# Performance work log

Measured on AMD Instinct MI355X. Metric: run time of the kernel, lower is better.

The kernel has to match this reference:

```python
import jax, jax.numpy as jnp
import numpy as np

B, S, D = 2, 2048, 1024
E, K, DFF = 8, 2, 4 * 1024
EPS_GATE = 1e-8
EPS_LN = 1e-5


def setup_inputs() -> dict:
    key = jax.random.key(0)
    ks = jax.random.split(key, 4)
    scaled = lambda k, shape, fan: (jax.random.normal(k, shape, jnp.float32) / np.sqrt(fan).astype(np.float32))
    return {
        "x": jax.random.normal(ks[0], (B, S, D), jnp.float32),
        "Wg": scaled(ks[1], (D, E), D),
        "bg": jnp.zeros((E,), jnp.float32),
        "W1": scaled(ks[2], (E, D, DFF), D),
        "b1": jnp.zeros((E, DFF), jnp.float32),
        "W2": scaled(ks[3], (E, DFF, D), DFF),
        "b2": jnp.zeros((E, D), jnp.float32),
        "gamma": jnp.ones((D,), jnp.float32),
        "beta": jnp.zeros((D,), jnp.float32),
    }


def reference(x, Wg, bg, W1, b1, W2, b2, gamma, beta):
    b, s, d = x.shape
    xf = x.reshape(-1, d)                       # [T, D]
    T = xf.shape[0]
    num_experts = Wg.shape[1]

    # Gating: softmax over experts, top-k, renormalize selected weights.
    logits = xf @ Wg + bg                       # [T, E]
    w = jax.nn.softmax(logits, axis=-1)
    top_w, top_idx = jax.lax.top_k(w, K)        # [T, K]
    top_w = top_w / (top_w.sum(axis=-1, keepdims=True) + EPS_GATE)

    # Dense combine weights: cw[t, e] = renormalized weight if e selected else 0.
    cw = jnp.zeros((T, num_experts), xf.dtype).at[
        jnp.arange(T)[:, None], top_idx].add(top_w)

    # Expert FFNs (loop over small fixed expert count), weighted combine.
    out = jnp.zeros_like(xf)
    for e in range(num_experts):
        h = jax.nn.gelu(xf @ W1[e] + b1[e], approximate=False)  # [T, DFF]
        y = h @ W2[e] + b2[e]                                    # [T, D]
        out = out + cw[:, e:e + 1] * y

    # LayerNorm over the whole combined output (as in the torch module).
    mu = out.mean(axis=-1, keepdims=True)
    var = out.var(axis=-1, keepdims=True)
    out = (out - mu) / jnp.sqrt(var + EPS_LN) * gamma + beta
    return out.reshape(b, s, d)
```

## Files before the change

### kernel.cpp

```cpp
#include <hip/hip_runtime.h>
#include <hip/hip_bf16.h>

#define TOK  4096
#define DIMD 1024
#define NEXP 8
#define DFFN 4096
#define NSLOT   (TOK*2 + NEXP*128)
#define NRB128  ((TOK*2)/128 + NEXP)

typedef __attribute__((ext_vector_type(8))) short bf16x8;
typedef __attribute__((ext_vector_type(4))) float f32x4;

__device__ __forceinline__ unsigned short f2bf(float f){
  unsigned int u = __float_as_uint(f);
  unsigned int r = u + 0x7FFFu + ((u >> 16) & 1u);
  return (unsigned short)(r >> 16);
}

__device__ __forceinline__ float bf2f(unsigned short h){
  unsigned int u = ((unsigned int)h) << 16;
  return __uint_as_float(u);
}

__device__ __forceinline__ void gload_lds16(const void* g, void* l){
  __builtin_amdgcn_global_load_lds(
      (const __attribute__((address_space(1))) unsigned int*)g,
      (__attribute__((address_space(3))) unsigned int*)l, 16, 0, 0);
}

__global__ __launch_bounds__(256) void k_gate_tr(
    const float* __restrict__ x, const float* __restrict__ Wg,
    const float* __restrict__ bg, int* __restrict__ topidx,
    float* __restrict__ topw, int* __restrict__ pos, int* __restrict__ count,
    unsigned short* __restrict__ xb,
    const float* __restrict__ W1, unsigned short* __restrict__ w1t,
    const float* __restrict__ W2, unsigned short* __restrict__ w2t)
{
  if (blockIdx.x < 4096){
    int bid = blockIdx.x;
    const float* I; unsigned short* O; int R, C, r0, c0;
    if (bid < 2048){
      const int e = bid >> 8, rem = bid & 255;
      R = DIMD; C = DFFN;
      I = W1 + (size_t)e * R * C; O = w1t + (size_t)e * R * C;
      r0 = (rem >> 5) * 128; c0 = (rem & 31) * 128;
    } else {
      bid -= 2048;
      const int e = bid >> 8, rem = bid & 255;
      R = DFFN; C = DIMD;
      I = W2 + (size_t)e * R * C; O = w2t + (size_t)e * R * C;
      r0 = (rem >> 3) * 128; c0 = (rem & 7) * 128;
    }
    __shared__ alignas(16) unsigned short tile[128*128];
    const int tid = threadIdx.x;
    const int qw = tid & 31;
    const int rw = tid >> 5;
    #pragma unroll
    for (int it = 0; it < 16; ++it){
      const int r = it * 8 + rw;
      const float4 v = *(const float4*)(I + (size_t)(r0 + r) * C + c0 + qw * 4);
      ushort4 o;
      o.x = f2bf(v.x); o.y = f2bf(v.y); o.z = f2bf(v.z); o.w = f2bf(v.w);
      const int slot = qw ^ ((r >> 2) & 31);
      *(ushort4*)&tile[r * 128 + slot * 4] = o;
    }
    __syncthreads();
    const int p  = tid & 31;
    const int cb = tid >> 5;
    #pragma unroll
    for (int it = 0; it < 4; ++it){
      const int cg = cb * 4 + it;
      const int sl = (cg ^ p) * 4;
      const ushort4 a0 = *(const ushort4*)&tile[(4*p + 0) * 128 + sl];
      const ushort4 a1 = *(const ushort4*)&tile[(4*p + 1) * 128 + sl];
      const ushort4 a2 = *(const ushort4*)&tile[(4*p + 2) * 128 + sl];
      const ushort4 a3 = *(const ushort4*)&tile[(4*p + 3) * 128 + sl];
      ushort4 o;
      o.x = a0.x; o.y = a1.x; o.z = a2.x; o.w = a3.x;
      *(ushort4*)(O + (size_t)(c0 + 4*cg + 0) * R + r0 + 4*p) = o;
      o.x = a0.y; o.y = a1.y; o.z = a2.y; o.w = a3.y;
      *(ushort4*)(O + (size_t)(c0 + 4*cg + 1) * R + r0 + 4*p) = o;
      o.x = a0.z; o.y = a1.z; o.z = a2.z; o.w = a3.z;
      *(ushort4*)(O + (size_t)(c0 + 4*cg + 2) * R + r0 + 4*p) = o;
      o.x = a0.w; o.y = a1.w; o.z = a2.w; o.w = a3.w;
      *(ushort4*)(O + (size_t)(c0 + 4*cg + 3) * R + r0 + 4*p) = o;
    }
    return;
  }
  const int gb = blockIdx.x - 4096;
  const int wid = threadIdx.x >> 6, lane = threadIdx.x & 63;
  const int t = gb * 4 + wid;
  const float* xr = x + (size_t)t * DIMD;
  unsigned short* xbr = xb + (size_t)t * DIMD;
  float acc[NEXP] = {0.f,0.f,0.f,0.f,0.f,0.f,0.f,0.f};
  #pragma unroll
  for (int j = 0; j < DIMD/64; ++j){
    const int d = j*64 + lane;
    const float xv = xr[d];
    xbr[d] = f2bf(xv);
    const float4 wa = *(const float4*)(Wg + (size_t)d*NEXP);
    const float4 wb = *(const float4*)(Wg + (size_t)d*NEXP + 4);
    acc[0] += xv*wa.x; acc[1] += xv*wa.y; acc[2] += xv*wa.z; acc[3] += xv*wa.w;
    acc[4] += xv*wb.x; acc[5] += xv*wb.y; acc[6] += xv*wb.z; acc[7] += xv*wb.w;
  }
  #pragma unroll
  for (int e = 0; e < NEXP; ++e){
    float v = acc[e];
    #pragma unroll
    for (int o = 32; o > 0; o >>= 1) v += __shfl_xor(v, o);
    acc[e] = v;
  }
  if (lane == 0){
    float lg[NEXP], m = -1e30f;
    #pragma unroll
    for (int e = 0; e < NEXP; ++e){ lg[e] = acc[e] + bg[e]; m = fmaxf(m, lg[e]); }
    float p[NEXP], S = 0.f;
    #pragma unroll
    for (int e = 0; e < NEXP; ++e){ p[e] = expf(lg[e] - m); S += p[e]; }
    int e0 = 0;
    #pragma unroll
    for (int e = 1; e < NEXP; ++e) if (p[e] > p[e0]) e0 = e;
    int e1 = (e0 == 0) ? 1 : 0;
    #pragma unroll
    for (int e = 0; e < NEXP; ++e){
      if (e == e0 || e == e1) continue;
      if (p[e] > p[e1]) e1 = e;
    }
    const float denom = p[e0] + p[e1] + 1e-8f * S;
    const float w0 = p[e0] / denom, w1 = p[e1] / denom;
    const int p0 = atomicAdd(&count[e0], 1);
    const int p1 = atomicAdd(&count[e1], 1);
    topidx[t*2] = e0; topidx[t*2+1] = e1;
    topw[t*2] = w0;   topw[t*2+1] = w1;
    pos[t*2] = p0;    pos[t*2+1] = p1;
  }
}

__global__ __launch_bounds__(256) void k_scatter(
    const int* __restrict__ topidx, const int* __restrict__ pos,
    const int* __restrict__ count, int* __restrict__ slot_of, int* __restrict__ tok_of)
{
  int basee[NEXP]; int bacc = 0;
  #pragma unroll
  for (int q = 0; q < NEXP; ++q){
    basee[q] = bacc << 7;
    bacc += (count[q] + 127) >> 7;
  }
  const int t = blockIdx.x * 256 + threadIdx.x;
  #pragma unroll
  for (int k = 0; k < 2; ++k){
    const int e = topidx[t*2+k];
    const int g = basee[e] + pos[t*2+k];
    slot_of[t*2+k] = g;
    tok_of[g] = t;
  }
}

template<int KD, int KSLICES, int NT, int MODE, int WAVES, int BM, int BN, int MINW>
__global__ __launch_bounds__(WAVES*64, MINW) void k_gemm(
    const unsigned short* __restrict__ A, const unsigned short* __restrict__ Bt,
    const float* __restrict__ bias, const int* __restrict__ tok_of,
    const int* __restrict__ count,
    unsigned short* __restrict__ outH, unsigned short* __restrict__ outY,
    unsigned short* __restrict__ outY1)
{
  const int by = blockIdx.y;
  int e = -1, b0 = 0;
  #pragma unroll
  for (int q = 0; q < NEXP; ++q){
    const int nb = (count[q] + 127) >> 7;
    if (e < 0){ if (by < b0 + nb) e = q; else b0 += nb; }
  }
  if (e < 0) return;
  const int ct = blockIdx.x;
  const int ks = (KSLICES == 1) ? 0 : blockIdx.z;
  constexpr int KSL = KD / KSLICES;
  const int kbase = ks * KSL;
  const int row0 = by * 128;
  constexpr int T   = WAVES * 64;
  constexpr int RA  = BM*8 / T;
  constexpr int RB  = BN*8 / T;
  constexpr int WN  = BN / 64;
  constexpr int WM  = WAVES / WN;
  constexpr int MR  = BM / WM / 16;
  __shared__ alignas(16) unsigned short sA[BM*64];
  __shared__ alignas(16) unsigned short sB[BN*64];
  const int tid = threadIdx.x, wid = tid >> 6, lane = tid & 63;

  const unsigned short* aptr[RA];
  #pragma unroll
  for (int i = 0; i < RA; ++i){
    const int s = i*T + tid;
    const int row = s >> 3;
    const int c = (s & 7) ^ (row & 7);
    size_t arow;
    if (MODE == 1) arow = (size_t)tok_of[row0 + row] * KD;
    else           arow = (size_t)(row0 + row) * KD;
    aptr[i] = A + arow + kbase + c*8;
  }
  const unsigned short* bptr[RB];
  #pragma unroll
  for (int i = 0; i < RB; ++i){
    const int s = i*T + tid;
    const int row = s >> 3;
    const int c = (s & 7) ^ (row & 7);
    bptr[i] = Bt + ((size_t)e*NT + ct*BN + row) * KD + kbase + c*8;
  }

  f32x4 acc[MR][4] = {};
  const int wr = wid / WN, wc = wid % WN;

  int aoff[MR][2], boff[4][2];
  #pragma unroll
  for (int m = 0; m < MR; ++m){
    #pragma unroll
    for (int s = 0; s < 2; ++s){
      const int rowA = wr*(MR*16) + m*16 + (lane & 15);
      aoff[m][s] = rowA*64 + (((s*4) + (lane >> 4)) ^ (rowA & 7))*8;
    }
  }
  #pragma unroll
  for (int n = 0; n < 4; ++n){
    #pragma unroll
    for (int s = 0; s < 2; ++s){
      const int rowB = wc*64 + n*16 + (lane & 15);
      boff[n][s] = rowB*64 + (((s*4) + (lane >> 4)) ^ (rowB & 7))*8;
    }
  }

  for (int k0 = 0; k0 < KSL; k0 += 64){
    #pragma unroll
    for (int i = 0; i < RA; ++i)
      gload_lds16(aptr[i] + k0, &sA[(i*T + tid - lane)*8]);
    #pragma unroll
    for (int i = 0; i < RB; ++i)
      gload_lds16(bptr[i] + k0, &sB[(i*T + tid - lane)*8]);
    __syncthreads();
    #pragma unroll
    for (int s = 0; s < 2; ++s){
      bf16x8 af[MR], bfr[4];
      #pragma unroll
      for (int m = 0; m < MR; ++m) af[m] = *(const bf16x8*)&sA[aoff[m][s]];
      #pragma unroll
      for (int n = 0; n < 4; ++n) bfr[n] = *(const bf16x8*)&sB[boff[n][s]];
      #pragma unroll
      for (int m = 0; m < MR; ++m)
        #pragma unroll
        for (int n = 0; n < 4; ++n)
          acc[m][n] = __builtin_amdgcn_mfma_f32_16x16x32_bf16(af[m], bfr[n], acc[m][n], 0, 0, 0);
    }
    __syncthreads();
  }

  const float* be = bias + (size_t)e * NT;
  unsigned short* outYs = (ks == 0) ? outY : outY1;
  #pragma unroll
  for (int m = 0; m < MR; ++m){
    #pragma unroll
    for (int n = 0; n < 4; ++n){
      #pragma unroll
      for (int j = 0; j < 4; ++j){
        const int rl = wr*(MR*16) + m*16 + ((lane >> 4) << 2) + j;
        const int ng = ct*BN + wc*64 + n*16 + (lane & 15);
        const size_t orow = (size_t)(row0 + rl) * NT + ng;
        if (MODE == 1){
          const float u = acc[m][n][j] + be[ng];
          float y = 0.7978845608028654f * (u + 0.044715f * u * u * u);
          y = fminf(fmaxf(y, -15.f), 15.f);
          const float ex = __expf(2.f * y);
          const float th = (ex - 1.f) / (ex + 1.f);
          outH[orow] = f2bf(0.5f * u * (1.f + th));
        } else {
          outYs[orow] = f2bf(acc[m][n][j] + ((ks == 0) ? be[ng] : 0.f));
        }
      }
    }
  }
}

__global__ __launch_bounds__(256) void k_combine_ln(
    const unsigned short* __restrict__ Ys0, const unsigned short* __restrict__ Ys1,
    const int* __restrict__ slot_of,
    const float* __restrict__ topw, const float* __restrict__ gamma,
    const float* __restrict__ beta, float* __restrict__ out)
{
  const int t = blockIdx.x;
  const int g0 = slot_of[t*2], g1 = slot_of[t*2+1];
  const float w0 = topw[t*2], w1 = topw[t*2+1];
  const int c = threadIdx.x;
  const ushort4 a0 = *(const ushort4*)(Ys0 + (size_t)g0*DIMD + c*4);
  const ushort4 a1 = *(const ushort4*)(Ys1 + (size_t)g0*DIMD + c*4);
  const ushort4 b0 = *(const ushort4*)(Ys0 + (size_t)g1*DIMD + c*4);
  const ushort4 b1 = *(const ushort4*)(Ys1 + (size_t)g1*DIMD + c*4);
  float4 v;
  v.x = w0*(bf2f(a0.x)+bf2f(a1.x)) + w1*(bf2f(b0.x)+bf2f(b1.x));
  v.y = w0*(bf2f(a0.y)+bf2f(a1.y)) + w1*(bf2f(b0.y)+bf2f(b1.y));
  v.z = w0*(bf2f(a0.z)+bf2f(a1.z)) + w1*(bf2f(b0.z)+bf2f(b1.z));
  v.w = w0*(bf2f(a0.w)+bf2f(a1.w)) + w1*(bf2f(b0.w)+bf2f(b1.w));
  float s  = v.x + v.y + v.z + v.w;
  float ss = v.x*v.x + v.y*v.y + v.z*v.z + v.w*v.w;
  #pragma unroll
  for (int o = 32; o > 0; o >>= 1){ s += __shfl_xor(s, o); ss += __shfl_xor(ss, o); }
  __shared__ float red[8];
  const int wid = threadIdx.x >> 6, lane = threadIdx.x & 63;
  if (lane == 0){ red[wid] = s; red[4 + wid] = ss; }
  __syncthreads();
  const float S  = red[0] + red[1] + red[2] + red[3];
  const float SS = red[4] + red[5] + red[6] + red[7];
  const float mu  = S * (1.f/DIMD);
  const float var = SS * (1.f/DIMD) - mu*mu;
  const float inv = rsqrtf(var + 1e-5f);
  const float4 gm = *(const float4*)(gamma + c*4);
  const float4 bt = *(const float4*)(beta + c*4);
  float4 o;
  o.x = (v.x - mu)*inv*gm.x + bt.x;
  o.y = (v.y - mu)*inv*gm.y + bt.y;
  o.z = (v.z - mu)*inv*gm.z + bt.z;
  o.w = (v.w - mu)*inv*gm.w + bt.w;
  *(float4*)(out + (size_t)t*DIMD + c*4) = o;
}

extern "C" void kernel_launch(void* const* d_in, const int* in_sizes, int n_in,
                              void* d_out, int out_size, void* d_ws, size_t ws_size,
                              hipStream_t stream)
{
  const float* x     = (const float*)d_in[0];
  const float* Wg    = (const float*)d_in[1];
  const float* bg    = (const float*)d_in[2];
  const float* W1    = (const float*)d_in[3];
  const float* b1    = (const float*)d_in[4];
  const float* W2    = (const float*)d_in[5];
  const float* b2    = (const float*)d_in[6];
  const float* gamma = (const float*)d_in[7];
  const float* beta  = (const float*)d_in[8];
  float* out = (float*)d_out;

  char* ws = (char*)d_ws;
  size_t off = 0;
  auto alloc = [&](size_t b){ char* p = ws + off; off += (b + 255) & ~(size_t)255; return p; };
  unsigned short* xb  = (unsigned short*)alloc((size_t)TOK*DIMD*2);
  unsigned short* w1t = (unsigned short*)alloc((size_t)NEXP*DFFN*DIMD*2);
  unsigned short* w2t = (unsigned short*)alloc((size_t)NEXP*DIMD*DFFN*2);
  unsigned short* Hs  = (unsigned short*)alloc((size_t)NSLOT*DFFN*2);
  int*   topidx  = (int*)alloc(TOK*2*4);
  float* topw    = (float*)alloc(TOK*2*4);
  int*   pos     = (int*)alloc(TOK*2*4);
  int*   slot_of = (int*)alloc(TOK*2*4);
  int*   tok_of  = (int*)alloc(NSLOT*4);
  int*   count   = (int*)alloc(256);
  unsigned short* Ys0b = (unsigned short*)w1t;
  unsigned short* Ys1b = Ys0b + (size_t)NSLOT*DIMD;

  (void)hipMemsetAsync(count, 0, NEXP*sizeof(int), stream);
  (void)hipMemsetAsync(tok_of, 0, NSLOT*sizeof(int), stream);
  k_gate_tr<<<5120, 256, 0, stream>>>(x, Wg, bg, topidx, topw, pos, count, xb,
                                      W1, w1t, W2, w2t);
  k_scatter<<<TOK/256, 256, 0, stream>>>(topidx, pos, count, slot_of, tok_of);
  k_gemm<DIMD, 1, DFFN, 1, 8, 128, 256, 4><<<dim3(DFFN/256, NRB128), 512, 0, stream>>>(
      xb, w1t, b1, tok_of, count, Hs, nullptr, nullptr);
  k_gemm<DFFN, 2, DIMD, 2, 8, 128, 256, 4><<<dim3(DIMD/256, NRB128, 2), 512, 0, stream>>>(
      Hs, w2t, b2, tok_of, count, nullptr, Ys0b, Ys1b);
  k_combine_ln<<<TOK, 256, 0, stream>>>(Ys0b, Ys1b, slot_of, topw, gamma, beta, out);
}
```

Before: 409.6 us.

## Move W2 transpose-convert into first expert GEMM launch as extra blocks

```diff
diff --git a/kernel.cpp b/kernel.cpp
--- a/kernel.cpp
+++ b/kernel.cpp
@@ -28,29 +28,20 @@
       (__attribute__((address_space(3))) unsigned int*)l, 16, 0, 0);
 }
 
-__global__ __launch_bounds__(256) void k_gate_tr(
+__global__ __launch_bounds__(256) void k_gate_trw1(
     const float* __restrict__ x, const float* __restrict__ Wg,
     const float* __restrict__ bg, int* __restrict__ topidx,
     float* __restrict__ topw, int* __restrict__ pos, int* __restrict__ count,
     unsigned short* __restrict__ xb,
-    const float* __restrict__ W1, unsigned short* __restrict__ w1t,
-    const float* __restrict__ W2, unsigned short* __restrict__ w2t)
-{
-  if (blockIdx.x < 4096){
-    int bid = blockIdx.x;
-    const float* I; unsigned short* O; int R, C, r0, c0;
-    if (bid < 2048){
-      const int e = bid >> 8, rem = bid & 255;
-      R = DIMD; C = DFFN;
-      I = W1 + (size_t)e * R * C; O = w1t + (size_t)e * R * C;
-      r0 = (rem >> 5) * 128; c0 = (rem & 31) * 128;
-    } else {
-      bid -= 2048;
-      const int e = bid >> 8, rem = bid & 255;
-      R = DFFN; C = DIMD;
-      I = W2 + (size_t)e * R * C; O = w2t + (size_t)e * R * C;
-      r0 = (rem >> 3) * 128; c0 = (rem & 7) * 128;
-    }
+    const float* __restrict__ W1, unsigned short* __restrict__ w1t)
+{
+  if (blockIdx.x < 2048){
+    const int bid = blockIdx.x;
+    const int e = bid >> 8, rem = bid & 255;
+    const int R = DIMD, C = DFFN;
+    const float* I = W1 + (size_t)e * R * C;
+    unsigned short* O = w1t + (size_t)e * R * C;
+    const int r0 = (rem >> 5) * 128, c0 = (rem & 31) * 128;
     __shared__ alignas(16) unsigned short tile[128*128];
     const int tid = threadIdx.x;
     const int qw = tid & 31;
@@ -87,7 +78,7 @@
     }
     return;
   }
-  const int gb = blockIdx.x - 4096;
+  const int gb = blockIdx.x - 2048;
   const int wid = threadIdx.x >> 6, lane = threadIdx.x & 63;
   const int t = gb * 4 + wid;
   const float* xr = x + (size_t)t * DIMD;
@@ -156,15 +147,60 @@
   }
 }
 
-template<int KD, int KSLICES, int NT, int MODE, int WAVES, int BM, int BN, int MINW>
+template<int KD, int KSLICES, int NT, int MODE, int WAVES, int BM, int BN, int MINW, int TRW2>
 __global__ __launch_bounds__(WAVES*64, MINW) void k_gemm(
     const unsigned short* __restrict__ A, const unsigned short* __restrict__ Bt,
     const float* __restrict__ bias, const int* __restrict__ tok_of,
     const int* __restrict__ count,
     unsigned short* __restrict__ outH, unsigned short* __restrict__ outY,
-    unsigned short* __restrict__ outY1)
-{
+    unsigned short* __restrict__ outY1,
+    const float* __restrict__ W2src, unsigned short* __restrict__ w2tdst)
+{
+  __shared__ alignas(16) unsigned short smem[BM*64 + BN*64];
   const int by = blockIdx.y;
+
+  if (TRW2 && by >= NRB128){
+    const int bid = (by - NRB128) * gridDim.x + blockIdx.x;
+    const int eT = bid >> 8, rem = bid & 255;
+    const int R = DFFN, C = DIMD;
+    const float* I = W2src + (size_t)eT * R * C;
+    unsigned short* O = w2tdst + (size_t)eT * R * C;
+    const int r0 = (rem >> 3) * 128, c0 = (rem & 7) * 128;
+    unsigned short* tile = smem;
+    const int tid = threadIdx.x;
+    const int qw = tid & 31, rw = tid >> 5;
+    #pragma unroll
+    for (int it = 0; it < 8; ++it){
+      const int r = it * 16 + rw;
+      const float4 v = *(const float4*)(I + (size_t)(r0 + r) * C + c0 + qw * 4);
+      ushort4 o;
+      o.x = f2bf(v.x); o.y = f2bf(v.y); o.z = f2bf(v.z); o.w = f2bf(v.w);
+      const int slot = qw ^ ((r >> 2) & 31);
+      *(ushort4*)&tile[r * 128 + slot * 4] = o;
+    }
+    __syncthreads();
+    const int p = tid & 31, cb = tid >> 5;
+    #pragma unroll
+    for (int it = 0; it < 2; ++it){
+      const int cg = cb * 2 + it;
+      const int sl = (cg ^ p) * 4;
+      const ushort4 a0 = *(const ushort4*)&tile[(4*p + 0) * 128 + sl];
+      const ushort4 a1 = *(const ushort4*)&tile[(4*p + 1) * 128 + sl];
+      const ushort4 a2 = *(const ushort4*)&tile[(4*p + 2) * 128 + sl];
+      const ushort4 a3 = *(const ushort4*)&tile[(4*p + 3) * 128 + sl];
+      ushort4 o;
+      o.x = a0.x; o.y = a1.x; o.z = a2.x; o.w = a3.x;
+      *(ushort4*)(O + (size_t)(c0 + 4*cg + 0) * R + r0 + 4*p) = o;
+      o.x = a0.y; o.y = a1.y; o.z = a2.y; o.w = a3.y;
+      *(ushort4*)(O + (size_t)(c0 + 4*cg + 1) * R + r0 + 4*p) = o;
+      o.x = a0.z; o.y = a1.z; o.z = a2.z; o.w = a3.z;
+      *(ushort4*)(O + (size_t)(c0 + 4*cg + 2) * R + r0 + 4*p) = o;
+      o.x = a0.w; o.y = a1.w; o.z = a2.w; o.w = a3.w;
+      *(ushort4*)(O + (size_t)(c0 + 4*cg + 3) * R + r0 + 4*p) = o;
+    }
+    return;
+  }
+
   int e = -1, b0 = 0;
   #pragma unroll
   for (int q = 0; q < NEXP; ++q){
@@ -183,8 +219,8 @@
   constexpr int WN  = BN / 64;
   constexpr int WM  = WAVES / WN;
   constexpr int MR  = BM / WM / 16;
-  __shared__ alignas(16) unsigned short sA[BM*64];
-  __shared__ alignas(16) unsigned short sB[BN*64];
+  unsigned short* sA = smem;
+  unsigned short* sB = smem + BM*64;
   const int tid = threadIdx.x, wid = tid >> 6, lane = tid & 63;
 
   const unsigned short* aptr[RA];
@@ -353,12 +389,11 @@
 
   (void)hipMemsetAsync(count, 0, NEXP*sizeof(int), stream);
   (void)hipMemsetAsync(tok_of, 0, NSLOT*sizeof(int), stream);
-  k_gate_tr<<<5120, 256, 0, stream>>>(x, Wg, bg, topidx, topw, pos, count, xb,
-                                      W1, w1t, W2, w2t);
+  k_gate_trw1<<<3072, 256, 0, stream>>>(x, Wg, bg, topidx, topw, pos, count, xb, W1, w1t);
   k_scatter<<<TOK/256, 256, 0, stream>>>(topidx, pos, count, slot_of, tok_of);
-  k_gemm<DIMD, 1, DFFN, 1, 8, 128, 256, 4><<<dim3(DFFN/256, NRB128), 512, 0, stream>>>(
-      xb, w1t, b1, tok_of, count, Hs, nullptr, nullptr);
-  k_gemm<DFFN, 2, DIMD, 2, 8, 128, 256, 4><<<dim3(DIMD/256, NRB128, 2), 512, 0, stream>>>(
-      Hs, w2t, b2, tok_of, count, nullptr, Ys0b, Ys1b);
+  k_gemm<DIMD, 1, DFFN, 1, 8, 128, 256, 4, 1><<<dim3(DFFN/256, NRB128 + 128), 512, 0, stream>>>(
+      xb, w1t, b1, tok_of, count, Hs, nullptr, nullptr, W2, w2t);
+  k_gemm<DFFN, 2, DIMD, 2, 8, 128, 256, 4, 0><<<dim3(DIMD/256, NRB128, 2), 512, 0, stream>>>(
+      Hs, w2t, b2, tok_of, count, nullptr, Ys0b, Ys1b, nullptr, nullptr);
   k_combine_ln<<<TOK, 256, 0, stream>>>(Ys0b, Ys1b, slot_of, topw, gamma, beta, out);
 }
```

Result: no change. 403.8 us (-1.4%).
